# Performance work log

Measured on AMD Instinct MI355X. Metric: run time of the kernel, lower is better.

## Reference

```python
import jax, jax.numpy as jnp
import numpy as np

# configuration (mirrors global `args` in the original code)
N_USER = 20000
N_ITEM = 20000
N = N_USER + N_ITEM            # total nodes; N*N < 2^31 so int32 hashing is safe
N_EDGES = 2_560_000
MASK_DEPTH = 2
KEEP_RATE = 0.5
N_SEEDS = 2000


def setup_inputs() -> dict:
    key = jax.random.key(0)
    k1, k2, k3 = jax.random.split(key, 3)
    rows = jax.random.randint(k1, (N_EDGES,), 0, N, dtype=jnp.int32)
    cols = jax.random.randint(k2, (N_EDGES,), 0, N, dtype=jnp.int32)
    vals = jnp.ones((N_EDGES,), jnp.float32)  # adj._values(); only its length is used
    seeds = jax.random.randint(k3, (N_SEEDS,), 0, N, dtype=jnp.int32)
    return {"rows": rows, "cols": cols, "vals": vals, "seeds": seeds}


def reference(rows, cols, vals, seeds):
    """Faithful vectorized translation of RandomMaskSubgraphs.forward.

    The per-seed python loop over edges is equivalent (in its final effect) to:
    per BFS level, drop every still-alive edge incident to the current seed set,
    and take the endpoints of dropped edges as the next seed set.
    Returns (enc_rows, enc_cols, enc_vals, dec_rows, dec_cols, dec_vals).
    Removed encoder edges carry value 0 (zero-value sparse entries == absent).
    """
    E = rows.shape[0]
    key = jax.random.key(1)
    kS, kR, kC = jax.random.split(key, 3)

    alive = jnp.ones(E, dtype=bool)                     # edges not yet masked
    seed_mask = jnp.zeros(N, dtype=bool).at[seeds].set(True)
    mask_nodes = seed_mask                               # union of maskNodes list
    cur = seed_mask
    for i in range(MASK_DEPTH):
        # membership test: edge incident to any current seed (single gather pass)
        hit = alive & (cur[rows] | cur[cols])
        alive = alive & ~hit
        if i != MASK_DEPTH - 1:
            # endpoints of masked edges become next frontier (scatter dedup)
            h = hit.astype(jnp.int32)
            touched = (jnp.zeros(N, jnp.int32).at[rows].add(h).at[cols].add(h)) > 0
            mask_nodes = mask_nodes | touched
            cur = touched

    # random keep-nodes augmentation
    samp_num = int(N * KEEP_RATE)
    samp = jax.random.randint(kS, (samp_num,), 0, N, dtype=jnp.int32)
    mask_nodes = mask_nodes.at[samp].set(True)

    # encoderAdj = normalizeAdj(sparse(ones on remaining edges))
    deg = jax.ops.segment_sum(alive.astype(jnp.float32), rows, num_segments=N)
    dinv = jnp.power(deg + 1e-12, -0.5)
    enc_vals = alive.astype(jnp.float32) * dinv[rows] * dinv[cols]

    # decoderAdj: random pairs among masked nodes + self loops + remaining edges,
    # deduplicated via integer hash row*N + col (fits int32 since N*N < 2^31)
    mask_idx = jnp.nonzero(mask_nodes)[0].astype(jnp.int32)
    tem_num = int(mask_idx.shape[0])
    tem_rows = mask_idx[jax.random.randint(kR, (E,), 0, tem_num)]
    tem_cols = mask_idx[jax.random.randint(kC, (E,), 0, tem_num)]
    ar = jnp.arange(N, dtype=jnp.int32)
    alive_rows = rows[alive]
    alive_cols = cols[alive]
    new_rows = jnp.concatenate([tem_rows, tem_cols, ar, alive_rows])
    new_cols = jnp.concatenate([tem_cols, tem_rows, ar, alive_cols])
    hash_val = jnp.unique(new_rows * N + new_cols)
    dec_cols = hash_val % N
    dec_rows = hash_val // N
    dec_vals = jnp.ones(dec_rows.shape[0], jnp.float32)

    return rows, cols, enc_vals, dec_rows, dec_cols, dec_vals
```

## Files before the change

kernel.cpp:

```cpp
#include <hip/hip_runtime.h>
#include <stdint.h>


#define NN 40000
#define SAMPN (NN / 2)
#define WORDS 1250
#define SWORDS 40
#define NB 1024
#define RPB 40
#define CAP 8192
#define CURSTRIDE 4
#define EPB 2816
#define NE (EPB / 256)
#define SELFPB 44
#define SCAP (3 * EPB + SELFPB)

__host__ __device__ __forceinline__ void tf2x32(unsigned k0, unsigned k1,
                                                unsigned x0, unsigned x1,
                                                unsigned &o0, unsigned &o1) {
  unsigned ks2 = k0 ^ k1 ^ 0x1BD11BDAu;
  x0 += k0; x1 += k1;
#define TFR(r) { x0 += x1; x1 = (x1 << (r)) | (x1 >> (32 - (r))); x1 ^= x0; }
  TFR(13) TFR(15) TFR(26) TFR(6)
  x0 += k1;  x1 += ks2 + 1u;
  TFR(17) TFR(29) TFR(16) TFR(24)
  x0 += ks2; x1 += k0 + 2u;
  TFR(13) TFR(15) TFR(26) TFR(6)
  x0 += k0;  x1 += k1 + 3u;
  TFR(17) TFR(29) TFR(16) TFR(24)
  x0 += k1;  x1 += ks2 + 4u;
  TFR(13) TFR(15) TFR(26) TFR(6)
  x0 += ks2; x1 += k0 + 5u;
#undef TFR
  o0 = x0; o1 = x1;
}

__device__ __forceinline__ unsigned jrand(unsigned a, unsigned b, unsigned c,
                                          unsigned d, unsigned e, unsigned span) {
  unsigned x0, x1, y0, y1;
  tf2x32(a, b, 0u, e, x0, x1);
  unsigned hi = x0 ^ x1;
  tf2x32(c, d, 0u, e, y0, y1);
  unsigned lo = y0 ^ y1;
  unsigned mult = 65536u % span;
  mult = (mult * mult) % span;
  return ((hi % span) * mult + (lo % span)) % span;
}

__global__ void k_zero16(uint4 *p, int n16) {
  int i = blockIdx.x * blockDim.x + threadIdx.x;
  if (i < n16) p[i] = make_uint4(0u, 0u, 0u, 0u);
}
__global__ void k_seed_samp(const int *seeds, int ns, unsigned char *cur,
                            unsigned char *mask_bfs,
                            unsigned a, unsigned b, unsigned c, unsigned d) {
  int i = blockIdx.x * blockDim.x + threadIdx.x;
  if (i < ns) { int s = seeds[i]; cur[s] = 1; mask_bfs[s] = 1; }
  if (i < SAMPN) {
    unsigned idx = jrand(a, b, c, d, (unsigned)i, (unsigned)NN);
    mask_bfs[idx] = 1;
  }
}
__global__ void k_level0(const int *rows, const int *cols, int E,
                         const unsigned char *cur, unsigned char *alive,
                         unsigned char *touched, unsigned char *mask_bfs) {
  int e = blockIdx.x * blockDim.x + threadIdx.x;
  if (e >= E) return;
  int r = rows[e], c = cols[e];
  if (cur[r] | cur[c]) {
    alive[e] = 0;
    touched[r] = 1; touched[c] = 1;
    mask_bfs[r] = 1; mask_bfs[c] = 1;
  } else alive[e] = 1;
}
__global__ void k_level1_deg(const int *rows, const int *cols, int E,
                             const unsigned char *touched, unsigned char *alive,
                             int *deg) {
  int e = blockIdx.x * blockDim.x + threadIdx.x;
  if (e >= E) return;
  if (alive[e]) {
    int r = rows[e];
    if (touched[r] | touched[cols[e]]) alive[e] = 0;
    else atomicAdd(&deg[r], 1);
  }
}
__global__ void k_enc(const int *rows, const int *cols, const unsigned char *alive,
                      const int *deg, int E, float *out) {
  int e = blockIdx.x * blockDim.x + threadIdx.x;
  if (e >= E) return;
  int r = rows[e], c = cols[e];
  float v = 0.0f;
  if (alive[e]) {
    float xr = (float)deg[r] + 1e-12f;
    float xc = (float)deg[c] + 1e-12f;
    float dr = (float)(1.0 / sqrt((double)xr));
    float dc = (float)(1.0 / sqrt((double)xc));
    v = dr * dc;
  }
  out[e] = (float)r;
  out[E + e] = (float)c;
  out[2 * E + e] = v;
}

__global__ __launch_bounds__(1024) void k_scan_mask(const unsigned char *flags,
                                                    unsigned short *mask_idx,
                                                    int *tem_num) {
  __shared__ int wsum[16];
  const unsigned *f = (const unsigned *)flags;
  int tid = threadIdx.x, lane = tid & 63, wid = tid >> 6;
  int base = tid * 10;
  unsigned u[10];
  int cnt = 0;
  for (int j = 0; j < 10; j++) {
    int i = base + j;
    u[j] = (i < 10000) ? f[i] : 0u;
    cnt += __popc(u[j]);
  }
  int x = cnt;
  for (int d = 1; d < 64; d <<= 1) {
    int y = __shfl_up(x, d, 64);
    if (lane >= d) x += y;
  }
  if (lane == 63) wsum[wid] = x;
  __syncthreads();
  if (wid == 0) {
    int v = (lane < 16) ? wsum[lane] : 0;
    int y = v;
    for (int d = 1; d < 16; d <<= 1) {
      int z = __shfl_up(y, d, 64);
      if (lane >= d) y += z;
    }
    if (lane < 16) wsum[lane] = y - v;
  }
  __syncthreads();
  int off = wsum[wid] + (x - cnt);
  for (int j = 0; j < 10; j++) {
    int i = base + j;
    unsigned v = u[j];
    while (v) {
      int byte = (__ffs(v) - 1) >> 3;
      v &= v - 1;
      mask_idx[off++] = (unsigned short)(i * 4 + byte);
    }
  }
  if (tid == 1023) *tem_num = off;
}

__global__ __launch_bounds__(256) void k_append(
    const int *rows, const int *cols, const unsigned char *alive,
    const unsigned short *mask_idx, const int *tem_num, int *cursors,
    unsigned *bucketmem,
    unsigned ra, unsigned rb, unsigned rc, unsigned rd,
    unsigned ca, unsigned cb, unsigned cc, unsigned cd, int E) {
  __shared__ unsigned sorted[SCAP];
  __shared__ int cnt[NB];
  __shared__ unsigned short ofs[NB];
  __shared__ int ntot_s;
  int tid = threadIdx.x, lane = tid & 63, wid = tid >> 6;
  int e0 = blockIdx.x * EPB;
  int i0 = blockIdx.x * SELFPB;
  int i1 = i0 + SELFPB; if (i1 > NN) i1 = NN;
  unsigned span = (unsigned)*tem_num;
  const unsigned NOPE = 0xFFFFFFFFu;

  unsigned tval[NE], aval[NE];

  for (int i = tid; i < NB; i += 256) cnt[i] = 0;
  __syncthreads();
#pragma unroll
  for (int k = 0; k < NE; k++) {
    int e = e0 + k * 256 + tid;
    if (e < E) {
      unsigned iR = jrand(ra, rb, rc, rd, (unsigned)e, span);
      unsigned iC = jrand(ca, cb, cc, cd, (unsigned)e, span);
      unsigned tr = (unsigned)mask_idx[iR], tc = (unsigned)mask_idx[iC];
      tval[k] = (tr << 16) | tc;
      atomicAdd(&cnt[tr / RPB], 1);
      atomicAdd(&cnt[tc / RPB], 1);
      if (alive[e]) {
        unsigned r = (unsigned)rows[e];
        aval[k] = (r << 16) | (unsigned)cols[e];
        atomicAdd(&cnt[r / RPB], 1);
      } else aval[k] = NOPE;
    } else { tval[k] = NOPE; aval[k] = NOPE; }
  }
  for (int i = i0 + tid; i < i1; i += 256) atomicAdd(&cnt[i / RPB], 1);
  __syncthreads();
  if (wid == 0) {
    int carry = 0;
    for (int c8 = 0; c8 < 16; c8++) {
      int v = cnt[c8 * 64 + lane];
      int x = v;
      for (int d = 1; d < 64; d <<= 1) {
        int y = __shfl_up(x, d, 64);
        if (lane >= d) x += y;
      }
      ofs[c8 * 64 + lane] = (unsigned short)(carry + x - v);
      carry += __shfl(x, 63, 64);
    }
    if (lane == 0) ntot_s = carry;
  }
  __syncthreads();
  for (int i = tid; i < NB; i += 256) cnt[i] = ofs[i];
  __syncthreads();
#pragma unroll
  for (int k = 0; k < NE; k++) {
    unsigned v = tval[k];
    if (v != NOPE) {
      unsigned tr = v >> 16, tc = v & 0xFFFFu;
      int p1 = atomicAdd(&cnt[tr / RPB], 1);
      sorted[p1] = v;
      int p2 = atomicAdd(&cnt[tc / RPB], 1);
      sorted[p2] = (tc << 16) | tr;
      unsigned a = aval[k];
      if (a != NOPE) {
        int p3 = atomicAdd(&cnt[(a >> 16) / RPB], 1);
        sorted[p3] = a;
      }
    }
  }
  for (int i = i0 + tid; i < i1; i += 256) {
    int p = atomicAdd(&cnt[i / RPB], 1);
    sorted[p] = ((unsigned)i << 16) | (unsigned)i;
  }
  __syncthreads();
  int ntot = ntot_s;
  for (int b = tid; b < NB; b += 256) {
    int end = (b < NB - 1) ? (int)ofs[b + 1] : ntot;
    int len = end - (int)ofs[b];
    cnt[b] = len ? atomicAdd(&cursors[b * CURSTRIDE], len) : 0;
  }
  __syncthreads();
  for (int j = tid; j < ntot; j += 256) {
    unsigned item = sorted[j];
    unsigned r = item >> 16;
    unsigned b = r / RPB;
    unsigned lr = r - b * RPB;
    int idx = cnt[b] + (j - (int)ofs[b]);
    if (idx < CAP) bucketmem[b * CAP + idx] = (lr << 16) | (item & 0xFFFFu);
  }
}

__global__ __launch_bounds__(256) void k_dedup(unsigned *bucketmem,
                                               const int *cursors, int *uniq_cnt) {
  int b = blockIdx.x;
  int rowbase = b * RPB;
  if (rowbase >= NN) { if (threadIdx.x == 0) uniq_cnt[b] = 0; return; }

  __shared__ unsigned short arr[CAP];
  __shared__ int cnt[RPB];
  __shared__ int rowend[RPB];
  __shared__ int curs[RPB];
  __shared__ int rowoff[RPB];
  __shared__ unsigned bm[4][WORDS];
  __shared__ unsigned sm[4][SWORDS];

  int tid = threadIdx.x, lane = tid & 63, wid = tid >> 6;
  int n = cursors[b * CURSTRIDE]; if (n > CAP) n = CAP;
  const unsigned *src = bucketmem + (size_t)b * CAP;

  for (int i = tid; i < RPB; i += 256) cnt[i] = 0;
  __syncthreads();
  for (int j = tid; j < n; j += 256) atomicAdd(&cnt[src[j] >> 16], 1);
  __syncthreads();
  if (tid == 0) {
    int s = 0;
    for (int r = 0; r < RPB; r++) { curs[r] = s; s += cnt[r]; rowend[r] = s; }
  }
  __syncthreads();
  for (int j = tid; j < n; j += 256) {
    unsigned v = src[j];
    int p = atomicAdd(&curs[v >> 16], 1);
    arr[p] = (unsigned short)v;
  }
  for (int w = lane; w < WORDS; w += 64) bm[wid][w] = 0u;
  if (lane < SWORDS) sm[wid][lane] = 0u;
  __syncthreads();

  for (int r = wid; r < RPB; r += 4) {
    int s1 = rowend[r], s0 = s1 - cnt[r];
    for (int j = s0 + lane; j < s1; j += 64) {
      unsigned c = arr[j];
      atomicOr(&bm[wid][c >> 5], 1u << (c & 31));
      atomicOr(&sm[wid][c >> 10], 1u << ((c >> 5) & 31));
    }
    unsigned s = (lane < SWORDS) ? sm[wid][lane] : 0u;
    int m = 0;
    unsigned t = s;
    while (t) {
      int w = (lane << 5) + (__ffs(t) - 1);
      t &= t - 1;
      m += __popc(bm[wid][w]);
    }
    int x = m;
    for (int d = 1; d < 64; d <<= 1) {
      int y = __shfl_up(x, d, 64);
      if (lane >= d) x += y;
    }
    int u = __shfl(x, 63, 64);
    int pos = s0 + (x - m);
    t = s;
    while (t) {
      int w = (lane << 5) + (__ffs(t) - 1);
      t &= t - 1;
      unsigned mm = bm[wid][w];
      bm[wid][w] = 0u;
      while (mm) {
        int bit = __ffs(mm) - 1;
        mm &= mm - 1;
        arr[pos++] = (unsigned short)((w << 5) + bit);
      }
    }
    if (lane < SWORDS) sm[wid][lane] = 0u;
    if (lane == 0) cnt[r] = u;
  }
  __syncthreads();
  if (tid == 0) {
    int s = 0;
    for (int r = 0; r < RPB; r++) { rowoff[r] = s; s += cnt[r]; }
    uniq_cnt[b] = s;
  }
  __syncthreads();
  unsigned *dst = bucketmem + (size_t)b * CAP;
  for (int r = wid; r < RPB; r += 4) {
    int s0 = r ? rowend[r - 1] : 0;
    int u = cnt[r], o = rowoff[r];
    unsigned hashbase = (unsigned)(rowbase + r) * 40000u;
    for (int j = lane; j < u; j += 64)
      dst[o + j] = hashbase + (unsigned)arr[s0 + j];
  }
}

__global__ __launch_bounds__(256) void k_emit(const unsigned *bucketmem,
                                              const int *uniq_cnt, float *out,
                                              int E, int U) {
  __shared__ int part[4];
  int b = blockIdx.x;
  int tid = threadIdx.x, lane = tid & 63, wid = tid >> 6;
  int acc = 0;
  for (int i = tid; i < NB; i += 256)
    if (i < b) acc += uniq_cnt[i];
  for (int d = 1; d < 64; d <<= 1) acc += __shfl_xor(acc, d, 64);
  if (lane == 0) part[wid] = acc;
  __syncthreads();
  int ob = part[0] + part[1] + part[2] + part[3];
  int ub = uniq_cnt[b];
  const unsigned *src = bucketmem + (size_t)b * CAP;
  int base3 = 3 * E;
  for (int j = tid; j < ub; j += 256) {
    unsigned h = src[j];
    unsigned r = h / 40000u;
    unsigned c = h - r * 40000u;
    int idx = ob + j;
    if (idx < U) {
      out[base3 + idx] = (float)r;
      out[base3 + U + idx] = (float)c;
      out[base3 + 2 * U + idx] = 1.0f;
    }
  }
  if (b == NB - 1 && tid == 0) {
    int C = ob + ub;
    if (C != U) {
      int d = C - U; if (d < 0) d = -d; if (d > 60000) d = 60000;
      out[base3] = (float)(300000 + d);
    }
  }
}

extern "C" void kernel_launch(void *const *d_in, const int *in_sizes, int n_in,
                              void *d_out, int out_size, void *d_ws,
                              size_t ws_size, hipStream_t stream) {
  const int *rows = (const int *)d_in[0];
  const int *cols = (const int *)d_in[1];
  const int *seeds = (const int *)d_in[3];
  const int E = in_sizes[0];
  const int ns = in_sizes[3];
  float *out = (float *)d_out;
  const int U = (out_size - 3 * E) / 3;

  int *I = (int *)d_ws;
  int *deg = I;      I += NN;
  int *cursors = I;  I += NB * CURSTRIDE;
  int *uniq_cnt = I; I += NB;
  unsigned char *cur = (unsigned char *)I;
  unsigned char *touched = cur + NN;
  unsigned char *mask_bfs = touched + NN;
  size_t zero_bytes = (size_t)((char *)(mask_bfs + NN) - (char *)deg);
  int *J = (int *)(mask_bfs + NN);
  int *tem_num = J;  J += 1;
  J += 1;
  unsigned short *mask_idx = (unsigned short *)J;
  J += NN / 2;
  unsigned *bucketmem = (unsigned *)J; J += (size_t)NB * CAP;
  unsigned char *alive = (unsigned char *)J;

  unsigned F[3][2];
  tf2x32(0u, 1u, 0u, 0u, F[0][0], F[0][1]);
  tf2x32(0u, 1u, 0u, 1u, F[1][0], F[1][1]);
  tf2x32(0u, 1u, 0u, 2u, F[2][0], F[2][1]);
  unsigned K[3][4];
  for (int s = 0; s < 3; s++) {
    tf2x32(F[s][0], F[s][1], 0u, 0u, K[s][0], K[s][1]);
    tf2x32(F[s][0], F[s][1], 0u, 1u, K[s][2], K[s][3]);
  }

  dim3 b(256);
  int gE = (E + 255) / 256;
  int gSS = (SAMPN + 255) / 256;
  int gT = (E + EPB - 1) / EPB;
  int n16 = (int)(zero_bytes / 16);

  k_zero16<<<(n16 + 255) / 256, b, 0, stream>>>((uint4 *)deg, n16);
  k_seed_samp<<<gSS, b, 0, stream>>>(seeds, ns, cur, mask_bfs,
                                     K[0][0], K[0][1], K[0][2], K[0][3]);
  k_level0<<<gE, b, 0, stream>>>(rows, cols, E, cur, alive, touched, mask_bfs);
  k_level1_deg<<<gE, b, 0, stream>>>(rows, cols, E, touched, alive, deg);
  k_enc<<<gE, b, 0, stream>>>(rows, cols, alive, deg, E, out);
  k_scan_mask<<<1, 1024, 0, stream>>>(mask_bfs, mask_idx, tem_num);
  k_append<<<gT, b, 0, stream>>>(rows, cols, alive, mask_idx, tem_num,
                                 cursors, bucketmem,
                                 K[1][0], K[1][1], K[1][2], K[1][3],
                                 K[2][0], K[2][1], K[2][2], K[2][3], E);
  k_dedup<<<NB, b, 0, stream>>>(bucketmem, cursors, uniq_cnt);
  k_emit<<<NB, b, 0, stream>>>(bucketmem, uniq_cnt, out, E, U);
}
```

Baseline: 278.0 us.

## Fuse encoder output into append kernel, halve bucket count, pack hashes by shift

Removes the separate k_enc pass and computes the normalized encoder values inside k_append, which already reads rows, cols and alive. This avoids a second full read of the edge arrays and one kernel launch. It also halves the number of dedup buckets (more rows per bucket, larger capacity) and replaces the row*40000 hash with a 16-bit shift pack, so decoding uses shifts instead of division. Larger buckets raise per-block shared-memory and work imbalance in dedup. Fusion also adds register pressure to k_append.

```diff
diff --git a/kernel.cpp b/kernel.cpp
--- a/kernel.cpp
+++ b/kernel.cpp
@@ -6,9 +6,9 @@
 #define SAMPN (NN / 2)
 #define WORDS 1250
 #define SWORDS 40
-#define NB 1024
-#define RPB 40
-#define CAP 8192
+#define NB 512
+#define RPB 79
+#define CAP 16384
 #define CURSTRIDE 4
 #define EPB 2816
 #define NE (EPB / 256)
@@ -84,23 +84,6 @@
     else atomicAdd(&deg[r], 1);
   }
 }
-__global__ void k_enc(const int *rows, const int *cols, const unsigned char *alive,
-                      const int *deg, int E, float *out) {
-  int e = blockIdx.x * blockDim.x + threadIdx.x;
-  if (e >= E) return;
-  int r = rows[e], c = cols[e];
-  float v = 0.0f;
-  if (alive[e]) {
-    float xr = (float)deg[r] + 1e-12f;
-    float xc = (float)deg[c] + 1e-12f;
-    float dr = (float)(1.0 / sqrt((double)xr));
-    float dc = (float)(1.0 / sqrt((double)xc));
-    v = dr * dc;
-  }
-  out[e] = (float)r;
-  out[E + e] = (float)c;
-  out[2 * E + e] = v;
-}
 
 __global__ __launch_bounds__(1024) void k_scan_mask(const unsigned char *flags,
                                                     unsigned short *mask_idx,
@@ -148,8 +131,8 @@
 
 __global__ __launch_bounds__(256) void k_append(
     const int *rows, const int *cols, const unsigned char *alive,
-    const unsigned short *mask_idx, const int *tem_num, int *cursors,
-    unsigned *bucketmem,
+    const int *deg, const unsigned short *mask_idx, const int *tem_num,
+    int *cursors, unsigned *bucketmem, float *out,
     unsigned ra, unsigned rb, unsigned rc, unsigned rd,
     unsigned ca, unsigned cb, unsigned cc, unsigned cd, int E) {
   __shared__ unsigned sorted[SCAP];
@@ -177,18 +160,27 @@
       tval[k] = (tr << 16) | tc;
       atomicAdd(&cnt[tr / RPB], 1);
       atomicAdd(&cnt[tc / RPB], 1);
+      int r = rows[e], c = cols[e];
+      float v = 0.0f;
       if (alive[e]) {
-        unsigned r = (unsigned)rows[e];
-        aval[k] = (r << 16) | (unsigned)cols[e];
-        atomicAdd(&cnt[r / RPB], 1);
+        aval[k] = ((unsigned)r << 16) | (unsigned)c;
+        atomicAdd(&cnt[(unsigned)r / RPB], 1);
+        float xr = (float)deg[r] + 1e-12f;
+        float xc = (float)deg[c] + 1e-12f;
+        float dr = (float)(1.0 / sqrt((double)xr));
+        float dc = (float)(1.0 / sqrt((double)xc));
+        v = dr * dc;
       } else aval[k] = NOPE;
+      out[e] = (float)r;
+      out[E + e] = (float)c;
+      out[2 * E + e] = v;
     } else { tval[k] = NOPE; aval[k] = NOPE; }
   }
   for (int i = i0 + tid; i < i1; i += 256) atomicAdd(&cnt[i / RPB], 1);
   __syncthreads();
   if (wid == 0) {
     int carry = 0;
-    for (int c8 = 0; c8 < 16; c8++) {
+    for (int c8 = 0; c8 < NB / 64; c8++) {
       int v = cnt[c8 * 64 + lane];
       int x = v;
       for (int d = 1; d < 64; d <<= 1) {
@@ -325,9 +317,9 @@
   for (int r = wid; r < RPB; r += 4) {
     int s0 = r ? rowend[r - 1] : 0;
     int u = cnt[r], o = rowoff[r];
-    unsigned hashbase = (unsigned)(rowbase + r) * 40000u;
+    unsigned rowpack = (unsigned)(rowbase + r) << 16;
     for (int j = lane; j < u; j += 64)
-      dst[o + j] = hashbase + (unsigned)arr[s0 + j];
+      dst[o + j] = rowpack | (unsigned)arr[s0 + j];
   }
 }
 
@@ -349,8 +341,8 @@
   int base3 = 3 * E;
   for (int j = tid; j < ub; j += 256) {
     unsigned h = src[j];
-    unsigned r = h / 40000u;
-    unsigned c = h - r * 40000u;
+    unsigned r = h >> 16;
+    unsigned c = h & 0xFFFFu;
     int idx = ob + j;
     if (idx < U) {
       out[base3 + idx] = (float)r;
@@ -415,10 +407,9 @@
                                      K[0][0], K[0][1], K[0][2], K[0][3]);
   k_level0<<<gE, b, 0, stream>>>(rows, cols, E, cur, alive, touched, mask_bfs);
   k_level1_deg<<<gE, b, 0, stream>>>(rows, cols, E, touched, alive, deg);
-  k_enc<<<gE, b, 0, stream>>>(rows, cols, alive, deg, E, out);
   k_scan_mask<<<1, 1024, 0, stream>>>(mask_bfs, mask_idx, tem_num);
-  k_append<<<gT, b, 0, stream>>>(rows, cols, alive, mask_idx, tem_num,
-                                 cursors, bucketmem,
+  k_append<<<gT, b, 0, stream>>>(rows, cols, alive, deg, mask_idx, tem_num,
+                                 cursors, bucketmem, out,
                                  K[1][0], K[1][1], K[1][2], K[1][3],
                                  K[2][0], K[2][1], K[2][2], K[2][3], E);
   k_dedup<<<NB, b, 0, stream>>>(bucketmem, cursors, uniq_cnt);
```

Result: slower. 295.4 us (+6.3%).
